# Kernel tuning notes

Hardware: AMD Instinct MI355X
Metric: run time of the kernel (lower is better)

## Reference

```python
import jax, jax.numpy as jnp
from jax import lax
import numpy as np

B, INP, WIDTH, OUTP, E, H = 32, 1024, 256, 1024, 8, 14
EPS = 1e-5


def setup_inputs() -> dict:
    key = jax.random.key(0)
    ks = jax.random.split(key, 12)
    n = lambda k, s, sc=0.05: jax.random.normal(k, s, jnp.float32) * sc
    return {
        "x": jax.random.normal(ks[0], (B, INP, H, H), jnp.float32),
        "w1": n(ks[1], (E, WIDTH, INP, 1, 1)),
        "w2": n(ks[2], (E, WIDTH, WIDTH, 3, 3)),
        "w3": n(ks[3], (E, OUTP, WIDTH, 1, 1)),
        "r1_w": n(ks[4], (INP, E)), "r1_b": jnp.zeros((E,), jnp.float32),
        "r2_w": n(ks[5], (WIDTH, E)), "r2_b": jnp.zeros((E,), jnp.float32),
        "r3_w": n(ks[6], (WIDTH, E)), "r3_b": jnp.zeros((E,), jnp.float32),
        "bn1_g": jax.random.uniform(ks[7], (WIDTH,), jnp.float32, 0.5, 1.5),
        "bn1_b": n(ks[8], (WIDTH,), 0.1),
        "bn1_m": jnp.zeros((WIDTH,), jnp.float32), "bn1_v": jnp.ones((WIDTH,), jnp.float32),
        "bn2_g": jax.random.uniform(ks[9], (WIDTH,), jnp.float32, 0.5, 1.5),
        "bn2_b": n(ks[10], (WIDTH,), 0.1),
        "bn2_m": jnp.zeros((WIDTH,), jnp.float32), "bn2_v": jnp.ones((WIDTH,), jnp.float32),
        "bn3_g": jax.random.uniform(ks[11], (OUTP,), jnp.float32, 0.5, 1.5),
        "bn3_b": jnp.zeros((OUTP,), jnp.float32),
        "bn3_m": jnp.zeros((OUTP,), jnp.float32), "bn3_v": jnp.ones((OUTP,), jnp.float32),
    }


def _route(x, w, b):
    # global avg pool -> linear -> sigmoid : [B, E]
    return jax.nn.sigmoid(x.mean(axis=(2, 3)) @ w + b)


def _cond_conv(x, w, rw, stride=1, padding=0, dilation=1, groups=1):
    # x: [B,Cin,H,W]; w: [E,Cout,Cin/groups,kh,kw]; rw: [B,E]
    Bn, Cin, Hh, Ww = x.shape
    _, Cout, Cin_g, kh, kw = w.shape
    # per-sample expert-combined kernels, then batch-grouped conv
    cw = jnp.einsum('be,eoikl->boikl', rw, w).reshape(Bn * Cout, Cin_g, kh, kw)
    out = lax.conv_general_dilated(
        x.reshape(1, Bn * Cin, Hh, Ww), cw,
        window_strides=(stride, stride),
        padding=[(padding, padding), (padding, padding)],
        rhs_dilation=(dilation, dilation),
        feature_group_count=Bn * groups,
        dimension_numbers=('NCHW', 'OIHW', 'NCHW'))
    return out.reshape(Bn, Cout, out.shape[2], out.shape[3])


def _bn(x, g, b, m, v):
    inv = lax.rsqrt(v + EPS) * g
    return x * inv[None, :, None, None] + (b - m * inv)[None, :, None, None]


def reference(x, w1, w2, w3, r1_w, r1_b, r2_w, r2_b, r3_w, r3_b,
              bn1_g, bn1_b, bn1_m, bn1_v, bn2_g, bn2_b, bn2_m, bn2_v,
              bn3_g, bn3_b, bn3_m, bn3_v):
    identity = x
    rw1 = _route(x, r1_w, r1_b)
    out = jax.nn.relu(_bn(_cond_conv(x, w1, rw1), bn1_g, bn1_b, bn1_m, bn1_v))
    rw2 = _route(out, r2_w, r2_b)
    out = jax.nn.relu(_bn(_cond_conv(out, w2, rw2, stride=1, padding=1), bn2_g, bn2_b, bn2_m, bn2_v))
    rw3 = _route(out, r3_w, r3_b)
    out = _bn(_cond_conv(out, w3, rw3), bn3_g, bn3_b, bn3_m, bn3_v)
    return jax.nn.relu(out + identity)
```

## Files before the change

### kernel.cpp

```cpp
#include <hip/hip_runtime.h>
#include <hip/hip_bf16.h>

#define BB 32
#define INP 1024
#define WIDTH 256
#define OUTP 1024
#define NE 8
#define HW 196
#define HH 14
#define EPS 1e-5f

#define S1 (WIDTH * INP)
#define S2 (WIDTH * WIDTH * 9)
#define S3 (OUTP * WIDTH)

typedef __attribute__((ext_vector_type(8))) short bf16x8;
typedef __attribute__((ext_vector_type(4))) float f32x4;
typedef __attribute__((ext_vector_type(8))) unsigned short u16x8;


__device__ __forceinline__ unsigned short f2bf_bits(float f) {
    unsigned u = __float_as_uint(f);
    u += 0x7FFFu + ((u >> 16) & 1u);
    return (unsigned short)(u >> 16);
}
__device__ __forceinline__ float bf2f(unsigned short h) {
    return __uint_as_float((unsigned)h << 16);
}

#if defined(__has_builtin)
#if __has_builtin(__builtin_amdgcn_global_load_lds)
#define HAVE_GLL 1
#endif
#endif
__device__ __forceinline__ void gl2lds(const unsigned short* g, unsigned short* l,
                                       int lane) {
#ifdef HAVE_GLL
    __builtin_amdgcn_global_load_lds(
        (const __attribute__((address_space(1))) unsigned int*)(const void*)g,
        (__attribute__((address_space(3))) unsigned int*)(void*)l, 16, 0, 0);
#else
    *(u16x8*)(l + lane * 8) = *(const u16x8*)g;
#endif
}

__device__ __forceinline__ void block_route(
    const float* __restrict__ vec, const float* __restrict__ W,
    const float* __restrict__ bias, float scale, int C, int g,
    float* srw, int tid) {
    int wv = tid >> 6, lane = tid & 63;
    float p0[NE], p1[NE];
#pragma unroll
    for (int e = 0; e < NE; e++) { p0[e] = 0.f; p1[e] = 0.f; }
    const float* v0 = vec + (size_t)(g * 8 + wv * 2) * C;
    const float* v1 = v0 + C;
    for (int c = lane; c < C; c += 64) {
        float4 wa = *(const float4*)(W + c * 8);
        float4 wb = *(const float4*)(W + c * 8 + 4);
        float m0 = v0[c], m1 = v1[c];
        p0[0] += m0 * wa.x; p0[1] += m0 * wa.y; p0[2] += m0 * wa.z; p0[3] += m0 * wa.w;
        p0[4] += m0 * wb.x; p0[5] += m0 * wb.y; p0[6] += m0 * wb.z; p0[7] += m0 * wb.w;
        p1[0] += m1 * wa.x; p1[1] += m1 * wa.y; p1[2] += m1 * wa.z; p1[3] += m1 * wa.w;
        p1[4] += m1 * wb.x; p1[5] += m1 * wb.y; p1[6] += m1 * wb.z; p1[7] += m1 * wb.w;
    }
#pragma unroll
    for (int j = 1; j < 64; j <<= 1) {
#pragma unroll
        for (int e = 0; e < NE; e++) {
            p0[e] += __shfl_xor(p0[e], j, 64);
            p1[e] += __shfl_xor(p1[e], j, 64);
        }
    }
    if (lane == 0) {
#pragma unroll
        for (int e = 0; e < NE; e++) {
            srw[(wv * 2) * 8 + e] = 1.0f / (1.0f + expf(-(scale * p0[e] + bias[e])));
            srw[(wv * 2 + 1) * 8 + e] = 1.0f / (1.0f + expf(-(scale * p1[e] + bias[e])));
        }
    }
    __syncthreads();
}

__global__ __launch_bounds__(256) void pre_kernel(
    const float* __restrict__ x, unsigned short* __restrict__ xb,
    float* __restrict__ mean1,
    const float* __restrict__ w2, unsigned short* __restrict__ wb2) {
    __shared__ __align__(16) char smem[128 * 17 * 4];
    int blk = blockIdx.x, t = threadIdx.x;
    if (blk < 256) {
        float (*lt)[17] = (float(*)[17])smem;
        int b = blk >> 3, yq = blk & 7, c0 = yq * 128;
        int cr = t >> 1, half = t & 1;
        const float* src = x + ((size_t)(b * INP + c0 + cr)) * HW;
        float msum = 0.f;
        int j = t >> 4, nl = t & 15;
        for (int pg = 0; pg < 14; pg++) {
            int p0 = pg * 16 + half * 8;
            float vv[8];
            if (pg < 12) {
                float4 a = *(const float4*)(src + p0);
                float4 c = *(const float4*)(src + p0 + 4);
                vv[0] = a.x; vv[1] = a.y; vv[2] = a.z; vv[3] = a.w;
                vv[4] = c.x; vv[5] = c.y; vv[6] = c.z; vv[7] = c.w;
            } else {
#pragma unroll
                for (int i = 0; i < 8; i++) {
                    int p = p0 + i;
                    vv[i] = (p < HW) ? src[p] : 0.f;
                }
            }
#pragma unroll
            for (int i = 0; i < 8; i++) { msum += vv[i]; lt[cr][half * 8 + i] = vv[i]; }
            __syncthreads();
            unsigned short pk[8];
#pragma unroll
            for (int i = 0; i < 8; i++) pk[i] = f2bf_bits(lt[j * 8 + i][nl]);
            size_t tile = ((size_t)b * 14 + pg) * 32 + (size_t)(yq * 4 + (j >> 2));
            int lane = nl | ((j & 3) << 4);
            *(u16x8*)(xb + tile * 512 + lane * 8) = *(u16x8*)pk;
            __syncthreads();
        }
        float other = __shfl_xor(msum, 1, 64);
        if (half == 0) mean1[b * INP + c0 + cr] = (msum + other) * (1.0f / (float)HW);
    } else {
        unsigned short* lds = (unsigned short*)smem;
        int eo = blk - 256;
        const float* src = w2 + (size_t)eo * 2304 + (size_t)t * 9;
#pragma unroll
        for (int t9 = 0; t9 < 9; t9++) lds[t9 * 256 + t] = f2bf_bits(src[t9]);
        __syncthreads();
        unsigned short* dst = wb2 + (size_t)eo * 2304;
        for (int j = t; j < 288; j += 256)
            *(u16x8*)(dst + j * 8) = *(const u16x8*)(lds + j * 8);
    }
}

__global__ __launch_bounds__(256) void combine_cont_r(
    const float* __restrict__ w, const float* __restrict__ vec,
    const float* __restrict__ rW, const float* __restrict__ rB, float scale, int C,
    unsigned short* __restrict__ cw, int S, int Mt, int Kt) {
    __shared__ float srw[64];
    int tid = threadIdx.x, wv = tid >> 6, lane = tid & 63, ml = lane & 15, k8l = lane >> 4;
    int g = blockIdx.y;
    block_route(vec, rW, rB, scale, C, g, srw, tid);
    int kq = Kt >> 2;
    int mt = blockIdx.x / kq, kt = (blockIdx.x - mt * kq) * 4 + wv;
    int K = Kt * 32;
    const float* src = w + (size_t)(mt * 16 + ml) * K + kt * 32 + k8l * 8;
    float v[NE][8];
#pragma unroll
    for (int e = 0; e < NE; e++) {
        float4 a = *(const float4*)(src + (size_t)e * S);
        float4 c = *(const float4*)(src + (size_t)e * S + 4);
        v[e][0] = a.x; v[e][1] = a.y; v[e][2] = a.z; v[e][3] = a.w;
        v[e][4] = c.x; v[e][5] = c.y; v[e][6] = c.z; v[e][7] = c.w;
    }
    size_t dto = ((size_t)mt * Kt + kt) * 512 + (size_t)lane * 8;
    size_t bstr = (size_t)Mt * Kt * 512;
    for (int bl = 0; bl < 8; bl++) {
        int b = g * 8 + bl;
        float acc[8];
#pragma unroll
        for (int jj = 0; jj < 8; jj++) acc[jj] = 0.f;
#pragma unroll
        for (int e = 0; e < NE; e++) {
            float r = srw[bl * NE + e];
#pragma unroll
            for (int jj = 0; jj < 8; jj++) acc[jj] += r * v[e][jj];
        }
        u16x8 o;
#pragma unroll
        for (int jj = 0; jj < 8; jj++) o[jj] = f2bf_bits(acc[jj]);
        *(u16x8*)(cw + (size_t)b * bstr + dto) = o;
    }
}

__global__ __launch_bounds__(256) void combine_w2_r(
    const unsigned short* __restrict__ wb2, const float* __restrict__ vec,
    const float* __restrict__ rW, const float* __restrict__ rB, float scale,
    unsigned short* __restrict__ cw) {
    __shared__ float srw[64];
    int tid = threadIdx.x, wv = tid >> 6, lane = tid & 63, ol = lane & 15, g4 = lane >> 4;
    int g = blockIdx.y;
    block_route(vec, rW, rB, scale, 256, g, srw, tid);
    int ot = blockIdx.x / 18, kt = (blockIdx.x - ot * 18) * 4 + wv;
    const unsigned short* src = wb2 + (size_t)(ot * 16 + ol) * 2304 + kt * 32 + g4 * 8;
    float v[NE][8];
#pragma unroll
    for (int e = 0; e < NE; e++) {
        u16x8 raw = *(const u16x8*)(src + (size_t)e * S2);
#pragma unroll
        for (int jj = 0; jj < 8; jj++) v[e][jj] = bf2f(raw[jj]);
    }
    size_t dto = ((size_t)ot * 72 + kt) * 512 + (size_t)lane * 8;
    for (int bl = 0; bl < 8; bl++) {
        int b = g * 8 + bl;
        float acc[8];
#pragma unroll
        for (int jj = 0; jj < 8; jj++) acc[jj] = 0.f;
#pragma unroll
        for (int e = 0; e < NE; e++) {
            float r = srw[bl * NE + e];
#pragma unroll
            for (int jj = 0; jj < 8; jj++) acc[jj] += r * v[e][jj];
        }
        u16x8 out;
#pragma unroll
        for (int jj = 0; jj < 8; jj++) out[jj] = f2bf_bits(acc[jj]);
        *(u16x8*)(cw + (size_t)b * (16 * 72 * 512) + dto) = out;
    }
}

__device__ __forceinline__ void epilogue_act(
    const f32x4* acc, int b, int mt, int nt0, int nB, int lo, int g4,
    const float* __restrict__ g, const float* __restrict__ be,
    const float* __restrict__ mu, const float* __restrict__ var,
    unsigned short* __restrict__ actout, float* __restrict__ msum) {
    int c0 = mt * 16 + g4 * 4;
    float sc[4], sh[4];
#pragma unroll
    for (int r = 0; r < 4; r++) {
        float iv = rsqrtf(var[c0 + r] + EPS) * g[c0 + r];
        sc[r] = iv;
        sh[r] = be[c0 + r] - mu[c0 + r] * iv;
    }
    float ms[4] = {0.f, 0.f, 0.f, 0.f};
    int ktc = mt >> 1;
    int lanehi = ((mt * 2 + (g4 >> 1)) & 3) << 4;
#pragma unroll
    for (int t = 0; t < 4; t++) {
        if (t >= nB) break;
        int nt = nt0 + t;
        int n = nt * 16 + lo;
        float v[4];
#pragma unroll
        for (int r = 0; r < 4; r++) {
            float val = acc[t][r] * sc[r] + sh[r];
            val = fmaxf(val, 0.f);
            if (n >= HW) val = 0.f;
            v[r] = val;
            ms[r] += val;
        }
        unsigned p01 = (unsigned)f2bf_bits(v[0]) | ((unsigned)f2bf_bits(v[1]) << 16);
        unsigned p23 = (unsigned)f2bf_bits(v[2]) | ((unsigned)f2bf_bits(v[3]) << 16);
        size_t off = (((size_t)(b * 14 + nt)) * 8 + ktc) * 512 + (size_t)(lo | lanehi) * 8 + (g4 & 1) * 4;
        *(uint2*)(actout + off) = make_uint2(p01, p23);
    }
#pragma unroll
    for (int r = 0; r < 4; r++) {
        float s = ms[r];
        s += __shfl_xor(s, 1, 64);
        s += __shfl_xor(s, 2, 64);
        s += __shfl_xor(s, 4, 64);
        s += __shfl_xor(s, 8, 64);
        if (lo == 0) atomicAdd(&msum[b * 256 + c0 + r], s);
    }
}

__global__ __launch_bounds__(512) void gemm1_fused(
    const unsigned short* __restrict__ Bsw, const unsigned short* __restrict__ Asw,
    const float* __restrict__ g, const float* __restrict__ be,
    const float* __restrict__ mu, const float* __restrict__ var,
    unsigned short* __restrict__ actout, float* __restrict__ msum) {
    __shared__ __align__(16) unsigned short lAb[4][4 * 512];
    __shared__ __align__(16) unsigned short lBb[4][4 * 512];
    const int Kt = 32;
    int b = blockIdx.x, mh = blockIdx.y, z = blockIdx.z;
    int nt0 = (z < 3) ? z * 4 : 11;
    int nB = (z < 2) ? 4 : 3;
    int tid = threadIdx.x, wv = tid >> 6, grp = wv >> 2, wl = wv & 3;
    int lane = tid & 63, lo = lane & 15, g4 = lane >> 4;
    const unsigned short* Ab = Asw + (size_t)(b * 16 + mh * 4) * Kt * 512;
    const unsigned short* Bb = Bsw + (size_t)(b * 14 + nt0) * Kt * 512;
    f32x4 acc[4];
#pragma unroll
    for (int t = 0; t < 4; t++) acc[t] = {0.f, 0.f, 0.f, 0.f};

    auto stage = [&](int kt, unsigned short* lA, unsigned short* lB) {
        gl2lds(Ab + ((size_t)wl * Kt + kt) * 512 + lane * 8, lA + wl * 512, lane);
        if (wl < nB)
            gl2lds(Bb + ((size_t)wl * Kt + kt) * 512 + lane * 8, lB + wl * 512, lane);
    };
    auto compute = [&](const unsigned short* lA, const unsigned short* lB) {
        bf16x8 a0 = *(const bf16x8*)(lA + wl * 512 + lane * 8);
#pragma unroll
        for (int t = 0; t < 4; t++) {
            if (t >= nB) break;
            bf16x8 bt = *(const bf16x8*)(lB + t * 512 + lane * 8);
            acc[t] = __builtin_amdgcn_mfma_f32_16x16x32_bf16(a0, bt, acc[t], 0, 0, 0);
        }
    };

    stage(grp, lAb[grp], lBb[grp]);
    for (int kp = 0; kp < 16; kp++) {
        __syncthreads();
        if (kp < 15) {
            int s = 2 * kp + 2 + grp;
            stage(s, lAb[s & 3], lBb[s & 3]);
        }
        int c = (2 * kp + grp) & 3;
        compute(lAb[c], lBb[c]);
    }
    __syncthreads();
    float* red = (float*)&lBb[0][0];
    if (grp == 1) {
#pragma unroll
        for (int t = 0; t < 4; t++)
            *(f32x4*)(red + (((size_t)wl * 4 + t) * 64 + lane) * 4) = acc[t];
    }
    __syncthreads();
    if (grp == 0) {
#pragma unroll
        for (int t = 0; t < 4; t++) {
            f32x4 o = *(const f32x4*)(red + (((size_t)wl * 4 + t) * 64 + lane) * 4);
#pragma unroll
            for (int r = 0; r < 4; r++) acc[t][r] += o[r];
        }
        epilogue_act(acc, b, mh * 4 + wl, nt0, nB, lo, g4, g, be, mu, var, actout, msum);
    }
}

__global__ __launch_bounds__(512) void gemm2_fused(
    const unsigned short* __restrict__ act, const unsigned short* __restrict__ cw2,
    const unsigned short* __restrict__ zpad,
    const float* __restrict__ g, const float* __restrict__ be,
    const float* __restrict__ mu, const float* __restrict__ var,
    unsigned short* __restrict__ actout, float* __restrict__ msum) {
    __shared__ __align__(16) unsigned short lAb[4][4 * 512];
    __shared__ __align__(16) unsigned short lBb[4][4 * 512];
    int b = blockIdx.x, mh = blockIdx.y, z = blockIdx.z;
    int nt0 = (z < 3) ? z * 4 : 11;
    int nB = (z < 2) ? 4 : 3;
    int tid = threadIdx.x, wv = tid >> 6, grp = wv >> 2, wl = wv & 3;
    int lane = tid & 63, lo = lane & 15, g4 = lane >> 4;
    const unsigned short* Ab = cw2 + (size_t)(b * 16 + mh * 4) * 72 * 512;
    const unsigned short* actb = act + (size_t)b * 14 * 8 * 512;

    int p0 = (nt0 + wl) * 16 + lo;
    int py0 = p0 / HH, px0 = p0 - (p0 / HH) * HH;
    bool pv0 = (wl < nB) && (p0 < HW);

    f32x4 acc[4];
#pragma unroll
    for (int t = 0; t < 4; t++) acc[t] = {0.f, 0.f, 0.f, 0.f};

    auto stage = [&](int kt, unsigned short* lA, unsigned short* lB) {
        gl2lds(Ab + ((size_t)wl * 72 + kt) * 512 + lane * 8, lA + wl * 512, lane);
        if (wl < nB) {
            int t9 = kt >> 3;
            int dy = t9 / 3 - 1, dx = t9 - (t9 / 3) * 3 - 1;
            int itile = kt & 7;
            int sy = py0 + dy, sx = px0 + dx;
            bool ok = pv0 && sy >= 0 && sy < HH && sx >= 0 && sx < HH;
            int ns = sy * HH + sx;
            const unsigned short* gp = ok
                ? actb + ((size_t)(ns >> 4) * 8 + itile) * 512 + (size_t)((ns & 15) | (g4 << 4)) * 8
                : zpad;
            gl2lds(gp, lB + wl * 512, lane);
        }
    };
    auto compute = [&](const unsigned short* lA, const unsigned short* lB) {
        bf16x8 a0 = *(const bf16x8*)(lA + wl * 512 + lane * 8);
#pragma unroll
        for (int t = 0; t < 4; t++) {
            if (t >= nB) break;
            bf16x8 bt = *(const bf16x8*)(lB + t * 512 + lane * 8);
            acc[t] = __builtin_amdgcn_mfma_f32_16x16x32_bf16(a0, bt, acc[t], 0, 0, 0);
        }
    };

    stage(grp, lAb[grp], lBb[grp]);
    for (int kp = 0; kp < 36; kp++) {
        __syncthreads();
        if (kp < 35) {
            int s = 2 * kp + 2 + grp;
            stage(s, lAb[s & 3], lBb[s & 3]);
        }
        int c = (2 * kp + grp) & 3;
        compute(lAb[c], lBb[c]);
    }
    __syncthreads();
    float* red = (float*)&lBb[0][0];
    if (grp == 1) {
#pragma unroll
        for (int t = 0; t < 4; t++)
            *(f32x4*)(red + (((size_t)wl * 4 + t) * 64 + lane) * 4) = acc[t];
    }
    __syncthreads();
    if (grp == 0) {
#pragma unroll
        for (int t = 0; t < 4; t++) {
            f32x4 o = *(const f32x4*)(red + (((size_t)wl * 4 + t) * 64 + lane) * 4);
#pragma unroll
            for (int r = 0; r < 4; r++) acc[t][r] += o[r];
        }
        epilogue_act(acc, b, mh * 4 + wl, nt0, nB, lo, g4, g, be, mu, var, actout, msum);
    }
}

__global__ __launch_bounds__(512) void gemm3_fused(
    const unsigned short* __restrict__ Bsw, const unsigned short* __restrict__ Asw,
    const float* __restrict__ g, const float* __restrict__ be,
    const float* __restrict__ mu, const float* __restrict__ var,
    const unsigned short* __restrict__ xb, float* __restrict__ out) {
    __shared__ __align__(16) unsigned short lAb[4][8 * 512];
    __shared__ __align__(16) unsigned short lBb[4][7 * 512];
    int b = blockIdx.x, y = blockIdx.y, mh = y >> 1, nh = y & 1;
    int tid = threadIdx.x, wv = tid >> 6, grp = wv >> 2, wl = wv & 3;
    int lane = tid & 63, lo = lane & 15, g4 = lane >> 4;
    const unsigned short* Ab = Asw + (size_t)(b * 64 + mh * 8) * 8 * 512;
    const unsigned short* Bb = Bsw + (size_t)(b * 14 + nh * 7) * 8 * 512;
    f32x4 acc0[7], acc1[7];
#pragma unroll
    for (int t = 0; t < 7; t++) { acc0[t] = {0.f, 0.f, 0.f, 0.f}; acc1[t] = {0.f, 0.f, 0.f, 0.f}; }

    auto stage = [&](int kt, unsigned short* lA, unsigned short* lB) {
        gl2lds(Ab + ((size_t)wl * 8 + kt) * 512 + lane * 8, lA + wl * 512, lane);
        gl2lds(Ab + ((size_t)(wl + 4) * 8 + kt) * 512 + lane * 8, lA + (wl + 4) * 512, lane);
        gl2lds(Bb + ((size_t)wl * 8 + kt) * 512 + lane * 8, lB + wl * 512, lane);
        if (wl < 3)
            gl2lds(Bb + ((size_t)(4 + wl) * 8 + kt) * 512 + lane * 8, lB + (4 + wl) * 512, lane);
    };
    auto compute = [&](const unsigned short* lA, const unsigned short* lB) {
        bf16x8 a0 = *(const bf16x8*)(lA + wl * 512 + lane * 8);
        bf16x8 a1 = *(const bf16x8*)(lA + (wl + 4) * 512 + lane * 8);
#pragma unroll
        for (int t = 0; t < 7; t++) {
            bf16x8 bt = *(const bf16x8*)(lB + t * 512 + lane * 8);
            acc0[t] = __builtin_amdgcn_mfma_f32_16x16x32_bf16(a0, bt, acc0[t], 0, 0, 0);
            acc1[t] = __builtin_amdgcn_mfma_f32_16x16x32_bf16(a1, bt, acc1[t], 0, 0, 0);
        }
    };

    stage(grp, lAb[grp], lBb[grp]);
    for (int kp = 0; kp < 4; kp++) {
        __syncthreads();
        if (kp < 3) {
            int s = 2 * kp + 2 + grp;
            stage(s, lAb[s & 3], lBb[s & 3]);
        }
        int c = (2 * kp + grp) & 3;
        compute(lAb[c], lBb[c]);
    }
    __syncthreads();
    float* red = (float*)&lBb[0][0];
    if (grp == 1) {
#pragma unroll
        for (int t = 0; t < 7; t++)
            *(f32x4*)(red + (((size_t)wl * 7 + t) * 64 + lane) * 4) = acc0[t];
    }
    __syncthreads();
    if (grp == 0) {
#pragma unroll
        for (int t = 0; t < 7; t++) {
            f32x4 o = *(const f32x4*)(red + (((size_t)wl * 7 + t) * 64 + lane) * 4);
#pragma unroll
            for (int r = 0; r < 4; r++) acc0[t][r] += o[r];
        }
    }
    __syncthreads();
    if (grp == 1) {
#pragma unroll
        for (int t = 0; t < 7; t++)
            *(f32x4*)(red + (((size_t)wl * 7 + t) * 64 + lane) * 4) = acc1[t];
    }
    __syncthreads();
    if (grp != 0) return;
#pragma unroll
    for (int t = 0; t < 7; t++) {
        f32x4 o = *(const f32x4*)(red + (((size_t)wl * 7 + t) * 64 + lane) * 4);
#pragma unroll
        for (int r = 0; r < 4; r++) acc1[t][r] += o[r];
    }

#pragma unroll
    for (int a = 0; a < 2; a++) {
        int mt = mh * 8 + wl + 4 * a;
        int c0 = mt * 16 + g4 * 4;
        float sc[4], sh[4];
#pragma unroll
        for (int r = 0; r < 4; r++) {
            float iv = rsqrtf(var[c0 + r] + EPS) * g[c0 + r];
            sc[r] = iv;
            sh[r] = be[c0 + r] - mu[c0 + r] * iv;
        }
        int ktc = mt >> 1;
        int lanehi = ((mt * 2 + (g4 >> 1)) & 3) << 4;
#pragma unroll
        for (int t = 0; t < 7; t++) {
            int nt = nh * 7 + t;
            int n = nt * 16 + lo;
            if (n >= HW) continue;
            const unsigned short* xr = xb + (((size_t)(b * 14 + nt)) * 32 + ktc) * 512
                                       + (size_t)(lo | lanehi) * 8 + (g4 & 1) * 4;
            uint2 rv = *(const uint2*)xr;
            float res[4] = {bf2f((unsigned short)(rv.x & 0xffff)),
                            bf2f((unsigned short)(rv.x >> 16)),
                            bf2f((unsigned short)(rv.y & 0xffff)),
                            bf2f((unsigned short)(rv.y >> 16))};
            f32x4 av = a ? acc1[t] : acc0[t];
#pragma unroll
            for (int r = 0; r < 4; r++) {
                size_t oidx = ((size_t)(b * OUTP + c0 + r)) * HW + n;
                float val = av[r] * sc[r] + sh[r] + res[r];
                out[oidx] = fmaxf(val, 0.f);
            }
        }
    }
}

extern "C" void kernel_launch(void* const* d_in, const int* in_sizes, int n_in,
                              void* d_out, int out_size, void* d_ws, size_t ws_size,
                              hipStream_t stream) {
    const float* x    = (const float*)d_in[0];
    const float* w1   = (const float*)d_in[1];
    const float* w2   = (const float*)d_in[2];
    const float* w3   = (const float*)d_in[3];
    const float* r1_w = (const float*)d_in[4];
    const float* r1_b = (const float*)d_in[5];
    const float* r2_w = (const float*)d_in[6];
    const float* r2_b = (const float*)d_in[7];
    const float* r3_w = (const float*)d_in[8];
    const float* r3_b = (const float*)d_in[9];
    const float* bn1_g = (const float*)d_in[10];
    const float* bn1_b = (const float*)d_in[11];
    const float* bn1_m = (const float*)d_in[12];
    const float* bn1_v = (const float*)d_in[13];
    const float* bn2_g = (const float*)d_in[14];
    const float* bn2_b = (const float*)d_in[15];
    const float* bn2_m = (const float*)d_in[16];
    const float* bn2_v = (const float*)d_in[17];
    const float* bn3_g = (const float*)d_in[18];
    const float* bn3_b = (const float*)d_in[19];
    const float* bn3_m = (const float*)d_in[20];
    const float* bn3_v = (const float*)d_in[21];
    float* out = (float*)d_out;

    char* ws = (char*)d_ws;
    size_t off = 0;
    float* mean1 = (float*)(ws + off); off += (size_t)BB * INP * 4;
    float* msum2 = (float*)(ws + off); off += (size_t)BB * 256 * 4;
    float* msum3 = (float*)(ws + off); off += (size_t)BB * 256 * 4;
    unsigned short* zpad = (unsigned short*)(ws + off); off += 256;
    off = (off + 255) & ~(size_t)255;
    unsigned short* act1 = (unsigned short*)(ws + off); off += (size_t)BB * 14 * 8 * 512 * 2;
    unsigned short* act2 = (unsigned short*)(ws + off); off += (size_t)BB * 14 * 8 * 512 * 2;
    unsigned short* cw2 = (unsigned short*)(ws + off); off += (size_t)BB * 16 * 72 * 512 * 2;
    unsigned short* xb  = (unsigned short*)(ws + off); off += (size_t)BB * 14 * 32 * 512 * 2;
    unsigned short* wb2 = (unsigned short*)(ws + off); off += (size_t)S2 * NE * 2;
    unsigned short* cwX = (unsigned short*)(ws + off); off += (size_t)BB * S1 * 2;
    unsigned short* cw1 = cwX;
    unsigned short* cw3 = cwX;
    (void)ws_size;

    hipMemsetAsync(msum2, 0, (size_t)2 * BB * 256 * 4 + 256, stream);

    pre_kernel<<<2304, 256, 0, stream>>>(x, xb, mean1, w2, wb2);

    combine_cont_r<<<dim3(128, 4), 256, 0, stream>>>(w1, mean1, r1_w, r1_b, 1.0f, INP,
                                                     cw1, S1, 16, 32);
    gemm1_fused<<<dim3(BB, 4, 4), 512, 0, stream>>>(xb, cw1, bn1_g, bn1_b, bn1_m, bn1_v,
                                                    act1, msum2);

    combine_w2_r<<<dim3(288, 4), 256, 0, stream>>>(wb2, msum2, r2_w, r2_b,
                                                   1.0f / (float)HW, cw2);
    gemm2_fused<<<dim3(BB, 4, 4), 512, 0, stream>>>(act1, cw2, zpad, bn2_g, bn2_b,
                                                    bn2_m, bn2_v, act2, msum3);

    combine_cont_r<<<dim3(128, 4), 256, 0, stream>>>(w3, msum3, r3_w, r3_b,
                                                     1.0f / (float)HW, WIDTH,
                                                     cw3, S3, 64, 8);
    gemm3_fused<<<dim3(BB, 16), 512, 0, stream>>>(act2, cw3, bn3_g, bn3_b, bn3_m, bn3_v,
                                                  xb, out);
}
```

Measured before the change: 240.6 us.

## Retile gemm2, loop batch groups in combine kernels, fold memset into pre_kernel

Moves the zeroing of msum2/msum3/zpad from a separate hipMemsetAsync into pre_kernel, removing one launch. The combine kernels now run a single grid dimension and loop over the four batch groups. Each block loads the expert weights once and recomputes the routing per group, so the repeated weight reads across blockIdx.y go away, at the cost of a quarter of the blocks. gemm2 is retiled from 4 M-tiles × 4 N-quarters to 2 M-tiles × 7 N-tiles per block, sharing each staged activation tile across more output rows. An added __syncthreads at the start of block_route guards srw reuse between loop iterations.

```diff
diff --git a/kernel.cpp b/kernel.cpp
--- a/kernel.cpp
+++ b/kernel.cpp
@@ -48,6 +48,7 @@
     const float* __restrict__ vec, const float* __restrict__ W,
     const float* __restrict__ bias, float scale, int C, int g,
     float* srw, int tid) {
+    __syncthreads();
     int wv = tid >> 6, lane = tid & 63;
     float p0[NE], p1[NE];
 #pragma unroll
@@ -84,7 +85,9 @@
 __global__ __launch_bounds__(256) void pre_kernel(
     const float* __restrict__ x, unsigned short* __restrict__ xb,
     float* __restrict__ mean1,
-    const float* __restrict__ w2, unsigned short* __restrict__ wb2) {
+    const float* __restrict__ w2, unsigned short* __restrict__ wb2,
+    unsigned short* __restrict__ zpad,
+    float* __restrict__ msum2, float* __restrict__ msum3) {
     __shared__ __align__(16) char smem[128 * 17 * 4];
     int blk = blockIdx.x, t = threadIdx.x;
     if (blk < 256) {
@@ -125,6 +128,15 @@
     } else {
         unsigned short* lds = (unsigned short*)smem;
         int eo = blk - 256;
+        if (eo < 32) {
+            int idx = eo * 256 + t;
+            msum2[idx] = 0.f;
+            msum3[idx] = 0.f;
+            if (eo == 0 && t == 0) {
+                u16x8 z = {0, 0, 0, 0, 0, 0, 0, 0};
+                *(u16x8*)zpad = z;
+            }
+        }
         const float* src = w2 + (size_t)eo * 2304 + (size_t)t * 9;
 #pragma unroll
         for (int t9 = 0; t9 < 9; t9++) lds[t9 * 256 + t] = f2bf_bits(src[t9]);
@@ -141,8 +153,6 @@
     unsigned short* __restrict__ cw, int S, int Mt, int Kt) {
     __shared__ float srw[64];
     int tid = threadIdx.x, wv = tid >> 6, lane = tid & 63, ml = lane & 15, k8l = lane >> 4;
-    int g = blockIdx.y;
-    block_route(vec, rW, rB, scale, C, g, srw, tid);
     int kq = Kt >> 2;
     int mt = blockIdx.x / kq, kt = (blockIdx.x - mt * kq) * 4 + wv;
     int K = Kt * 32;
@@ -157,21 +167,24 @@
     }
     size_t dto = ((size_t)mt * Kt + kt) * 512 + (size_t)lane * 8;
     size_t bstr = (size_t)Mt * Kt * 512;
-    for (int bl = 0; bl < 8; bl++) {
-        int b = g * 8 + bl;
-        float acc[8];
-#pragma unroll
-        for (int jj = 0; jj < 8; jj++) acc[jj] = 0.f;
-#pragma unroll
-        for (int e = 0; e < NE; e++) {
-            float r = srw[bl * NE + e];
-#pragma unroll
-            for (int jj = 0; jj < 8; jj++) acc[jj] += r * v[e][jj];
-        }
-        u16x8 o;
-#pragma unroll
-        for (int jj = 0; jj < 8; jj++) o[jj] = f2bf_bits(acc[jj]);
-        *(u16x8*)(cw + (size_t)b * bstr + dto) = o;
+    for (int g = 0; g < 4; g++) {
+        block_route(vec, rW, rB, scale, C, g, srw, tid);
+        for (int bl = 0; bl < 8; bl++) {
+            int b = g * 8 + bl;
+            float acc[8];
+#pragma unroll
+            for (int jj = 0; jj < 8; jj++) acc[jj] = 0.f;
+#pragma unroll
+            for (int e = 0; e < NE; e++) {
+                float r = srw[bl * NE + e];
+#pragma unroll
+                for (int jj = 0; jj < 8; jj++) acc[jj] += r * v[e][jj];
+            }
+            u16x8 o;
+#pragma unroll
+            for (int jj = 0; jj < 8; jj++) o[jj] = f2bf_bits(acc[jj]);
+            *(u16x8*)(cw + (size_t)b * bstr + dto) = o;
+        }
     }
 }
 
@@ -181,8 +194,6 @@
     unsigned short* __restrict__ cw) {
     __shared__ float srw[64];
     int tid = threadIdx.x, wv = tid >> 6, lane = tid & 63, ol = lane & 15, g4 = lane >> 4;
-    int g = blockIdx.y;
-    block_route(vec, rW, rB, scale, 256, g, srw, tid);
     int ot = blockIdx.x / 18, kt = (blockIdx.x - ot * 18) * 4 + wv;
     const unsigned short* src = wb2 + (size_t)(ot * 16 + ol) * 2304 + kt * 32 + g4 * 8;
     float v[NE][8];
@@ -193,21 +204,24 @@
         for (int jj = 0; jj < 8; jj++) v[e][jj] = bf2f(raw[jj]);
     }
     size_t dto = ((size_t)ot * 72 + kt) * 512 + (size_t)lane * 8;
-    for (int bl = 0; bl < 8; bl++) {
-        int b = g * 8 + bl;
-        float acc[8];
-#pragma unroll
-        for (int jj = 0; jj < 8; jj++) acc[jj] = 0.f;
-#pragma unroll
-        for (int e = 0; e < NE; e++) {
-            float r = srw[bl * NE + e];
-#pragma unroll
-            for (int jj = 0; jj < 8; jj++) acc[jj] += r * v[e][jj];
-        }
-        u16x8 out;
-#pragma unroll
-        for (int jj = 0; jj < 8; jj++) out[jj] = f2bf_bits(acc[jj]);
-        *(u16x8*)(cw + (size_t)b * (16 * 72 * 512) + dto) = out;
+    for (int g = 0; g < 4; g++) {
+        block_route(vec, rW, rB, scale, 256, g, srw, tid);
+        for (int bl = 0; bl < 8; bl++) {
+            int b = g * 8 + bl;
+            float acc[8];
+#pragma unroll
+            for (int jj = 0; jj < 8; jj++) acc[jj] = 0.f;
+#pragma unroll
+            for (int e = 0; e < NE; e++) {
+                float r = srw[bl * NE + e];
+#pragma unroll
+                for (int jj = 0; jj < 8; jj++) acc[jj] += r * v[e][jj];
+            }
+            u16x8 out;
+#pragma unroll
+            for (int jj = 0; jj < 8; jj++) out[jj] = f2bf_bits(acc[jj]);
+            *(u16x8*)(cw + (size_t)b * (16 * 72 * 512) + dto) = out;
+        }
     }
 }
 
@@ -326,45 +340,57 @@
     const float* __restrict__ g, const float* __restrict__ be,
     const float* __restrict__ mu, const float* __restrict__ var,
     unsigned short* __restrict__ actout, float* __restrict__ msum) {
-    __shared__ __align__(16) unsigned short lAb[4][4 * 512];
-    __shared__ __align__(16) unsigned short lBb[4][4 * 512];
-    int b = blockIdx.x, mh = blockIdx.y, z = blockIdx.z;
-    int nt0 = (z < 3) ? z * 4 : 11;
-    int nB = (z < 2) ? 4 : 3;
+    __shared__ __align__(16) unsigned short lAb[4][2 * 512];
+    __shared__ __align__(16) unsigned short lBb[4][7 * 512];
+    int b = blockIdx.x, mh = blockIdx.y, nh = blockIdx.z;
     int tid = threadIdx.x, wv = tid >> 6, grp = wv >> 2, wl = wv & 3;
     int lane = tid & 63, lo = lane & 15, g4 = lane >> 4;
-    const unsigned short* Ab = cw2 + (size_t)(b * 16 + mh * 4) * 72 * 512;
+    const unsigned short* Ab = cw2 + (size_t)(b * 16 + mh * 2) * 72 * 512;
     const unsigned short* actb = act + (size_t)b * 14 * 8 * 512;
 
-    int p0 = (nt0 + wl) * 16 + lo;
-    int py0 = p0 / HH, px0 = p0 - (p0 / HH) * HH;
-    bool pv0 = (wl < nB) && (p0 < HW);
+    int stage_cnt = (wl == 3) ? 3 : ((wl == 2) ? 2 : 1);
+    int stage_b0 = (wl < 2) ? wl : ((wl == 2) ? 2 : 4);
+    int spy[3], spx[3];
+    bool spv[3];
+#pragma unroll
+    for (int j = 0; j < 3; j++) {
+        int p = (nh * 7 + stage_b0 + j) * 16 + lo;
+        spv[j] = p < HW;
+        spy[j] = p / HH;
+        spx[j] = p - (p / HH) * HH;
+    }
 
     f32x4 acc[4];
 #pragma unroll
     for (int t = 0; t < 4; t++) acc[t] = {0.f, 0.f, 0.f, 0.f};
 
     auto stage = [&](int kt, unsigned short* lA, unsigned short* lB) {
-        gl2lds(Ab + ((size_t)wl * 72 + kt) * 512 + lane * 8, lA + wl * 512, lane);
-        if (wl < nB) {
-            int t9 = kt >> 3;
-            int dy = t9 / 3 - 1, dx = t9 - (t9 / 3) * 3 - 1;
-            int itile = kt & 7;
-            int sy = py0 + dy, sx = px0 + dx;
-            bool ok = pv0 && sy >= 0 && sy < HH && sx >= 0 && sx < HH;
+        if (wl < 2)
+            gl2lds(Ab + ((size_t)wl * 72 + kt) * 512 + lane * 8, lA + wl * 512, lane);
+        int t9 = kt >> 3;
+        int dy = t9 / 3 - 1, dx = t9 - (t9 / 3) * 3 - 1;
+        int itile = kt & 7;
+#pragma unroll
+        for (int j = 0; j < 3; j++) {
+            if (j >= stage_cnt) break;
+            int sy = spy[j] + dy, sx = spx[j] + dx;
+            bool ok = spv[j] && sy >= 0 && sy < HH && sx >= 0 && sx < HH;
             int ns = sy * HH + sx;
             const unsigned short* gp = ok
                 ? actb + ((size_t)(ns >> 4) * 8 + itile) * 512 + (size_t)((ns & 15) | (g4 << 4)) * 8
                 : zpad;
-            gl2lds(gp, lB + wl * 512, lane);
+            gl2lds(gp, lB + (stage_b0 + j) * 512, lane);
         }
     };
     auto compute = [&](const unsigned short* lA, const unsigned short* lB) {
-        bf16x8 a0 = *(const bf16x8*)(lA + wl * 512 + lane * 8);
+        int msub = wl & 1, nr = wl >> 1;
+        int ntl = nr ? 3 : 4;
+        int bt0 = nr * 4;
+        bf16x8 a0 = *(const bf16x8*)(lA + msub * 512 + lane * 8);
 #pragma unroll
         for (int t = 0; t < 4; t++) {
-            if (t >= nB) break;
-            bf16x8 bt = *(const bf16x8*)(lB + t * 512 + lane * 8);
+            if (t >= ntl) break;
+            bf16x8 bt = *(const bf16x8*)(lB + (bt0 + t) * 512 + lane * 8);
             acc[t] = __builtin_amdgcn_mfma_f32_16x16x32_bf16(a0, bt, acc[t], 0, 0, 0);
         }
     };
@@ -388,13 +414,16 @@
     }
     __syncthreads();
     if (grp == 0) {
+        int msub = wl & 1, nr = wl >> 1;
+        int ntl = nr ? 3 : 4;
 #pragma unroll
         for (int t = 0; t < 4; t++) {
             f32x4 o = *(const f32x4*)(red + (((size_t)wl * 4 + t) * 64 + lane) * 4);
 #pragma unroll
             for (int r = 0; r < 4; r++) acc[t][r] += o[r];
         }
-        epilogue_act(acc, b, mh * 4 + wl, nt0, nB, lo, g4, g, be, mu, var, actout, msum);
+        epilogue_act(acc, b, mh * 2 + msub, nh * 7 + nr * 4, ntl, lo, g4,
+                     g, be, mu, var, actout, msum);
     }
 }
 
@@ -553,23 +582,21 @@
     unsigned short* cw3 = cwX;
     (void)ws_size;
 
-    hipMemsetAsync(msum2, 0, (size_t)2 * BB * 256 * 4 + 256, stream);
-
-    pre_kernel<<<2304, 256, 0, stream>>>(x, xb, mean1, w2, wb2);
-
-    combine_cont_r<<<dim3(128, 4), 256, 0, stream>>>(w1, mean1, r1_w, r1_b, 1.0f, INP,
-                                                     cw1, S1, 16, 32);
+    pre_kernel<<<2304, 256, 0, stream>>>(x, xb, mean1, w2, wb2, zpad, msum2, msum3);
+
+    combine_cont_r<<<128, 256, 0, stream>>>(w1, mean1, r1_w, r1_b, 1.0f, INP,
+                                            cw1, S1, 16, 32);
     gemm1_fused<<<dim3(BB, 4, 4), 512, 0, stream>>>(xb, cw1, bn1_g, bn1_b, bn1_m, bn1_v,
                                                     act1, msum2);
 
-    combine_w2_r<<<dim3(288, 4), 256, 0, stream>>>(wb2, msum2, r2_w, r2_b,
-                                                   1.0f / (float)HW, cw2);
-    gemm2_fused<<<dim3(BB, 4, 4), 512, 0, stream>>>(act1, cw2, zpad, bn2_g, bn2_b,
+    combine_w2_r<<<288, 256, 0, stream>>>(wb2, msum2, r2_w, r2_b,
+                                          1.0f / (float)HW, cw2);
+    gemm2_fused<<<dim3(BB, 8, 2), 512, 0, stream>>>(act1, cw2, zpad, bn2_g, bn2_b,
                                                     bn2_m, bn2_v, act2, msum3);
 
-    combine_cont_r<<<dim3(128, 4), 256, 0, stream>>>(w3, msum3, r3_w, r3_b,
-                                                     1.0f / (float)HW, WIDTH,
-                                                     cw3, S3, 64, 8);
+    combine_cont_r<<<128, 256, 0, stream>>>(w3, msum3, r3_w, r3_b,
+                                            1.0f / (float)HW, WIDTH,
+                                            cw3, S3, 64, 8);
     gemm3_fused<<<dim3(BB, 16), 512, 0, stream>>>(act2, cw3, bn3_g, bn3_b, bn3_m, bn3_v,
                                                   xb, out);
 }
```

New measurement: 290.5 us. +20.8%, slower.

## Deepen GEMM LDS pipeline with explicit vmcnt waits and fold memset into pre-kernel

Applied to the files above, without the earlier changes.

The gemm1 and gemm2 kernels grow their LDS ring from 4 to 8 stages and prefetch two k-steps ahead per group. The full __syncthreads is replaced by an explicit s_waitcnt vmcnt on the outstanding global-to-LDS loads followed by a bare s_barrier, so more loads stay in flight during the MFMA work. Separately, the hipMemsetAsync for msum2, msum3 and zpad is dropped and the zeroing is done inside pre_kernel, saving one launch. The larger LDS footprint may lower occupancy, and the hand-counted vmcnt values depend on how gl2lds expands, so a miscount could cause reads of stale LDS.

```diff
diff --git a/kernel.cpp b/kernel.cpp
--- a/kernel.cpp
+++ b/kernel.cpp
@@ -18,6 +18,8 @@
 typedef __attribute__((ext_vector_type(4))) float f32x4;
 typedef __attribute__((ext_vector_type(8))) unsigned short u16x8;
 
+
+#define VMCNT(n) asm volatile("s_waitcnt vmcnt(" #n ")" ::: "memory")
 
 __device__ __forceinline__ unsigned short f2bf_bits(float f) {
     unsigned u = __float_as_uint(f);
@@ -84,7 +86,9 @@
 __global__ __launch_bounds__(256) void pre_kernel(
     const float* __restrict__ x, unsigned short* __restrict__ xb,
     float* __restrict__ mean1,
-    const float* __restrict__ w2, unsigned short* __restrict__ wb2) {
+    const float* __restrict__ w2, unsigned short* __restrict__ wb2,
+    unsigned short* __restrict__ zpad,
+    float* __restrict__ msum2, float* __restrict__ msum3) {
     __shared__ __align__(16) char smem[128 * 17 * 4];
     int blk = blockIdx.x, t = threadIdx.x;
     if (blk < 256) {
@@ -125,6 +129,15 @@
     } else {
         unsigned short* lds = (unsigned short*)smem;
         int eo = blk - 256;
+        if (eo < 32) {
+            int idx = eo * 256 + t;
+            msum2[idx] = 0.f;
+            msum3[idx] = 0.f;
+            if (eo == 0 && t == 0) {
+                u16x8 z = {0, 0, 0, 0, 0, 0, 0, 0};
+                *(u16x8*)zpad = z;
+            }
+        }
         const float* src = w2 + (size_t)eo * 2304 + (size_t)t * 9;
 #pragma unroll
         for (int t9 = 0; t9 < 9; t9++) lds[t9 * 256 + t] = f2bf_bits(src[t9]);
@@ -262,8 +275,8 @@
     const float* __restrict__ g, const float* __restrict__ be,
     const float* __restrict__ mu, const float* __restrict__ var,
     unsigned short* __restrict__ actout, float* __restrict__ msum) {
-    __shared__ __align__(16) unsigned short lAb[4][4 * 512];
-    __shared__ __align__(16) unsigned short lBb[4][4 * 512];
+    __shared__ __align__(16) unsigned short lAb[8][4 * 512];
+    __shared__ __align__(16) unsigned short lBb[8][4 * 512];
     const int Kt = 32;
     int b = blockIdx.x, mh = blockIdx.y, z = blockIdx.z;
     int nt0 = (z < 3) ? z * 4 : 11;
@@ -276,12 +289,16 @@
 #pragma unroll
     for (int t = 0; t < 4; t++) acc[t] = {0.f, 0.f, 0.f, 0.f};
 
-    auto stage = [&](int kt, unsigned short* lA, unsigned short* lB) {
+    auto stage = [&](int kt) {
+        unsigned short* lA = lAb[kt & 7];
+        unsigned short* lB = lBb[kt & 7];
         gl2lds(Ab + ((size_t)wl * Kt + kt) * 512 + lane * 8, lA + wl * 512, lane);
         if (wl < nB)
             gl2lds(Bb + ((size_t)wl * Kt + kt) * 512 + lane * 8, lB + wl * 512, lane);
     };
-    auto compute = [&](const unsigned short* lA, const unsigned short* lB) {
+    auto compute = [&](int kt) {
+        const unsigned short* lA = lAb[kt & 7];
+        const unsigned short* lB = lBb[kt & 7];
         bf16x8 a0 = *(const bf16x8*)(lA + wl * 512 + lane * 8);
 #pragma unroll
         for (int t = 0; t < 4; t++) {
@@ -291,15 +308,19 @@
         }
     };
 
-    stage(grp, lAb[grp], lBb[grp]);
+    stage(grp);
+    stage(grp + 2);
     for (int kp = 0; kp < 16; kp++) {
-        __syncthreads();
-        if (kp < 15) {
-            int s = 2 * kp + 2 + grp;
-            stage(s, lAb[s & 3], lBb[s & 3]);
-        }
-        int c = (2 * kp + grp) & 3;
-        compute(lAb[c], lBb[c]);
+        int c = 2 * kp + grp;
+        if (c + 2 < 32) {
+            if (wl < nB) VMCNT(2); else VMCNT(1);
+        } else {
+            VMCNT(0);
+        }
+        __builtin_amdgcn_s_barrier();
+        int s = c + 4;
+        if (s < 32) stage(s);
+        compute(c);
     }
     __syncthreads();
     float* red = (float*)&lBb[0][0];
@@ -326,8 +347,8 @@
     const float* __restrict__ g, const float* __restrict__ be,
     const float* __restrict__ mu, const float* __restrict__ var,
     unsigned short* __restrict__ actout, float* __restrict__ msum) {
-    __shared__ __align__(16) unsigned short lAb[4][4 * 512];
-    __shared__ __align__(16) unsigned short lBb[4][4 * 512];
+    __shared__ __align__(16) unsigned short lAb[8][4 * 512];
+    __shared__ __align__(16) unsigned short lBb[8][4 * 512];
     int b = blockIdx.x, mh = blockIdx.y, z = blockIdx.z;
     int nt0 = (z < 3) ? z * 4 : 11;
     int nB = (z < 2) ? 4 : 3;
@@ -344,7 +365,9 @@
 #pragma unroll
     for (int t = 0; t < 4; t++) acc[t] = {0.f, 0.f, 0.f, 0.f};
 
-    auto stage = [&](int kt, unsigned short* lA, unsigned short* lB) {
+    auto stage = [&](int kt) {
+        unsigned short* lA = lAb[kt & 7];
+        unsigned short* lB = lBb[kt & 7];
         gl2lds(Ab + ((size_t)wl * 72 + kt) * 512 + lane * 8, lA + wl * 512, lane);
         if (wl < nB) {
             int t9 = kt >> 3;
@@ -359,7 +382,9 @@
             gl2lds(gp, lB + wl * 512, lane);
         }
     };
-    auto compute = [&](const unsigned short* lA, const unsigned short* lB) {
+    auto compute = [&](int kt) {
+        const unsigned short* lA = lAb[kt & 7];
+        const unsigned short* lB = lBb[kt & 7];
         bf16x8 a0 = *(const bf16x8*)(lA + wl * 512 + lane * 8);
 #pragma unroll
         for (int t = 0; t < 4; t++) {
@@ -369,15 +394,19 @@
         }
     };
 
-    stage(grp, lAb[grp], lBb[grp]);
+    stage(grp);
+    stage(grp + 2);
     for (int kp = 0; kp < 36; kp++) {
-        __syncthreads();
-        if (kp < 35) {
-            int s = 2 * kp + 2 + grp;
-            stage(s, lAb[s & 3], lBb[s & 3]);
-        }
-        int c = (2 * kp + grp) & 3;
-        compute(lAb[c], lBb[c]);
+        int c = 2 * kp + grp;
+        if (c + 2 < 72) {
+            if (wl < nB) VMCNT(2); else VMCNT(1);
+        } else {
+            VMCNT(0);
+        }
+        __builtin_amdgcn_s_barrier();
+        int s = c + 4;
+        if (s < 72) stage(s);
+        compute(c);
     }
     __syncthreads();
     float* red = (float*)&lBb[0][0];
@@ -553,9 +582,7 @@
     unsigned short* cw3 = cwX;
     (void)ws_size;
 
-    hipMemsetAsync(msum2, 0, (size_t)2 * BB * 256 * 4 + 256, stream);
-
-    pre_kernel<<<2304, 256, 0, stream>>>(x, xb, mean1, w2, wb2);
+    pre_kernel<<<2304, 256, 0, stream>>>(x, xb, mean1, w2, wb2, zpad, msum2, msum3);
 
     combine_cont_r<<<dim3(128, 4), 256, 0, stream>>>(w1, mean1, r1_w, r1_b, 1.0f, INP,
                                                      cw1, S1, 16, 32);
```

Measured after the change: 243.3 us (median of 2 runs). No clear change (+1.1%).
